# Performance work log

Hardware: AMD Instinct MI355X
Metric: run time of the kernel (lower is better)

The kernel has to match this reference:

```python
import jax, jax.numpy as jnp
import numpy as np

B, S, H, NH, DW, V, W, L, NL = 8, 512, 768, 12, 300, 100000, 256, 4, 2


def _make_word_index(seed=0):
    # contiguous, non-overlapping spans of length 1..L starting at pos 1,
    # zero-padded at the end (matches the `break` on (0,0) in the original).
    rng = np.random.default_rng(seed)
    wi = np.zeros((B, W, 2), np.int32)
    for b in range(B):
        pos, w = 1, 0
        while w < W and pos < S:
            n = int(rng.integers(1, L + 1))
            end = min(pos + n, S)
            wi[b, w] = (pos, end)
            pos, w = end, w + 1
    return jnp.asarray(wi)


def _lin(key, din, dout):
    kw, _ = jax.random.split(key)
    return jax.random.normal(kw, (din, dout), jnp.float32) * 0.02, jnp.zeros((dout,), jnp.float32)


def setup_inputs() -> dict:
    key = jax.random.key(0)
    ks = jax.random.split(key, 14)
    tbl = jax.random.normal(ks[2], (V + 1, DW), jnp.float32) * 0.1
    tbl = tbl.at[V].set(0.0)  # appended zero row for OOV/pad
    d = dict(
        sequence_output=jax.random.normal(ks[0], (B, S, H), jnp.float32),
        word_ids=jax.random.randint(ks[1], (B, W), 0, V),
        word_index=_make_word_index(),
        word_table=tbl,
        mix_lambda=jnp.asarray(0.5, jnp.float32),
        mu=jnp.asarray(0.5, jnp.float32),
    )
    d['dt_w'], d['dt_b'] = _lin(ks[3], DW, H)
    d['dr_w'], d['dr_b'] = _lin(ks[4], H, H)
    d['q_w'], d['q_b'] = _lin(ks[5], H, H)
    d['k_w'], d['k_b'] = _lin(ks[6], H, H)
    d['v_w'], d['v_b'] = _lin(ks[7], H, H)
    d['qi_w'], d['qi_b'] = _lin(ks[8], H, H)
    d['ki_w'], d['ki_b'] = _lin(ks[9], H, H)
    d['vi_w'], d['vi_b'] = _lin(ks[10], H, H)
    d['fus_w'], d['fus_b'] = _lin(ks[11], H, H)
    d['dense_w'], d['dense_b'] = _lin(ks[12], H, H)
    d['cls_w'], d['cls_b'] = _lin(ks[13], H, NL)
    return d


def _mhsa(x, wq, bq, wk, bk, wv, bv, bias=None):
    b, s, h = x.shape
    hd = h // NH
    q = (x @ wq + bq).reshape(b, s, NH, hd).transpose(0, 2, 1, 3)
    k = (x @ wk + bk).reshape(b, s, NH, hd).transpose(0, 2, 1, 3)
    v = (x @ wv + bv).reshape(b, s, NH, hd).transpose(0, 2, 1, 3)
    scores = jnp.einsum('bhqd,bhkd->bhqk', q, k) / jnp.sqrt(jnp.asarray(hd, x.dtype))
    if bias is not None:
        scores = scores + bias
    p = jax.nn.softmax(scores, axis=-1)
    return jnp.einsum('bhqk,bhkd->bhqd', p, v).transpose(0, 2, 1, 3).reshape(b, s, h)


def _forward(sequence_output, word_ids, word_index, word_table, dt_w, dt_b, dr_w, dr_b,
             mix_lambda, mu, q_w, q_b, k_w, k_b, v_w, v_b, qi_w, qi_b, ki_w, ki_b,
             vi_w, vi_b, fus_w, fus_b, dense_w, dense_b, cls_w, cls_b):
    x = sequence_output
    # word embedding -> dim_transform -> tanh -> dim_retain
    we = jnp.tanh(word_table[word_ids] @ dt_w + dt_b) @ dr_w + dr_b  # [B,W,H]
    starts, ends = word_index[..., 0], word_index[..., 1]
    n = ends - starts                     # word lengths, 0 for padding
    valid_w = n > 0
    lpos = jnp.arange(L)
    pos = jnp.clip(starts[..., None] + lpos, 0, S - 1)              # [B,W,L]
    cvalid = (lpos[None, None, :] < n[..., None]) & valid_w[..., None]
    bidx = jnp.arange(B)[:, None, None]
    # char-word cosine similarity (computed on the ORIGINAL sequence_output)
    xg = x[bidx, pos]                                               # [B,W,L,H]
    xn = xg / jnp.linalg.norm(xg, axis=-1, keepdims=True)
    wen = we / jnp.linalg.norm(we, axis=-1, keepdims=True)
    cos = jnp.sum(xn * wen[:, :, None, :], axis=-1)                 # [B,W,L]
    cos_m = jnp.where(cvalid, cos, -1e9)
    # add softmax(cos)-weighted word embedding onto chars (scatter-add)
    sm = jax.nn.softmax(cos_m, axis=-1) * cvalid
    x1 = x.at[bidx, pos].add(sm[..., None] * we[:, :, None, :])
    # ragged mix: most-important char (mic) per word
    mic = jnp.argmax(cos_m, axis=-1)                                # [B,W]
    x1g = x1[bidx, pos]                                             # [B,W,L,H]
    x_mic = x1g[jnp.arange(B)[:, None], jnp.arange(W)[None, :], mic]  # [B,W,H]
    sum_x = jnp.sum(x1g * cvalid[..., None], axis=2)                # [B,W,H]
    f = jnp.exp(mix_lambda - 1.0)
    a = (1.0 - f) / jnp.maximum(n - 1, 1).astype(x.dtype)           # [B,W]
    mix_other = (1.0 - a[..., None, None]) * x1g + a[..., None, None] * x_mic[:, :, None, :]
    mix_mic = f * x_mic + a[..., None] * (sum_x - x_mic)
    is_mic = lpos[None, None, :] == mic[:, :, None]
    newv = jnp.where(is_mic[..., None], mix_mic[:, :, None, :], mix_other)
    mixmask = (cvalid & (n > 1)[..., None])[..., None].astype(x.dtype)
    x_mix = x1.at[bidx, pos].add((newv - x1g) * mixmask)
    # importance attention mask: only mic (or the single char) columns visible
    keep_pos = jnp.where(n == 1, starts, jnp.clip(starts + mic, 0, S - 1))
    keep = jnp.zeros((B, S), bool).at[jnp.arange(B)[:, None], keep_pos].max(valid_w)
    bias = jnp.where(keep[:, None, None, :], 0.0, -jnp.inf).astype(x.dtype)  # [B,1,1,S]
    h1 = _mhsa(x_mix, q_w, q_b, k_w, k_b, v_w, v_b, None)
    h2 = _mhsa(x_mix, qi_w, qi_b, ki_w, ki_b, vi_w, vi_b, bias)
    fus = jnp.tanh((mu * h1 + (1.0 - mu) * h2) @ fus_w + fus_b)
    pooled = jnp.tanh(fus[:, 0] @ dense_w + dense_b)                # CLS pooling
    return pooled @ cls_w + cls_b                                   # [B,NL]


def reference(sequence_output, word_ids, word_index, word_table, dt_w, dt_b, dr_w, dr_b,
              mix_lambda, mu, q_w, q_b, k_w, k_b, v_w, v_b, qi_w, qi_b, ki_w, ki_b,
              vi_w, vi_b, fus_w, fus_b, dense_w, dense_b, cls_w, cls_b):
    return _forward(sequence_output, word_ids, word_index, word_table, dt_w, dt_b, dr_w, dr_b,
                    mix_lambda, mu, q_w, q_b, k_w, k_b, v_w, v_b, qi_w, qi_b, ki_w, ki_b,
                    vi_w, vi_b, fus_w, fus_b, dense_w, dense_b, cls_w, cls_b)
```

## Files before the change

### kernel.cpp

```cpp
#include <hip/hip_runtime.h>
#include <math.h>

#define NB 8
#define SS 512
#define HH 768
#define NHD 12
#define HDIM 64
#define DWD 300
#define WW 256
#define LL 4
#define KC 6

__device__ __forceinline__ float waveReduceSum(float v){
    #pragma unroll
    for(int o=32;o>0;o>>=1) v += __shfl_xor(v,o,64);
    return v;
}

__global__ __launch_bounds__(256) void k_embed1f(const float* __restrict__ table,
        const int* __restrict__ ids, const float* __restrict__ Wm,
        const float* __restrict__ bias, float* __restrict__ out,
        int* __restrict__ keep,
        const float* __restrict__ x, const float* __restrict__ qw,
        const float* __restrict__ qiw, float* __restrict__ qpart){
    int bid = blockIdx.x;
    int t = threadIdx.x;
    if(bid >= 400){
        int rb = bid - 400;
        int kc = rb % KC;
        int jt = (rb/KC) % 3;
        int b  = rb / (KC*3);
        int j = jt*256 + t;
        const float* x0 = x + (size_t)b*SS*HH;
        int i0 = kc*128;
        float a1=0.f, a2=0.f;
        for(int i=i0;i<i0+128;i++){
            float xv = x0[i];
            a1 += xv*qw[(size_t)i*HH+j];
            a2 += xv*qiw[(size_t)i*HH+j];
        }
        qpart[(((size_t)kc*NB + b)*2 + 0)*HH + j] = a1;
        qpart[(((size_t)kc*NB + b)*2 + 1)*HH + j] = a2;
        return;
    }
    if(bid >= 384){
        int i = (bid-384)*256 + t;
        if(i < NB*SS) keep[i] = 0;
        return;
    }
    const int K=300, NT=19;
    __shared__ float As[16][68];
    __shared__ float Bs[16][68];
    int bx = bid % 12;
    int by = bid / 12;
    int m0 = by*64, n0 = bx*64;
    int tm = t>>4, tn = t&15;
    int lm = t>>2, lk = (t&3)*4;
    int kk = t>>4, c4 = (t&15)*4;
    int row_id = ids[m0+lm];
    const float* arow = table + (size_t)row_id*DWD;
    float acc[4][4] = {};
    float4 av, bv;
    if(lk < K) av = *(const float4*)&arow[lk]; else av = make_float4(0,0,0,0);
    if(kk < K) bv = *(const float4*)&Wm[(size_t)kk*HH + n0 + c4]; else bv = make_float4(0,0,0,0);
    for(int kt=0;kt<NT;kt++){
        __syncthreads();
        As[lk+0][lm]=av.x; As[lk+1][lm]=av.y; As[lk+2][lm]=av.z; As[lk+3][lm]=av.w;
        *(float4*)&Bs[kk][c4] = bv;
        __syncthreads();
        if(kt+1 < NT){
            int k0 = (kt+1)*16;
            if(k0+lk < K) av = *(const float4*)&arow[k0+lk]; else av = make_float4(0,0,0,0);
            if(k0+kk < K) bv = *(const float4*)&Wm[(size_t)(k0+kk)*HH + n0 + c4]; else bv = make_float4(0,0,0,0);
        }
        #pragma unroll
        for(int k=0;k<16;k++){
            float4 a = *(const float4*)&As[k][tm*4];
            float4 b = *(const float4*)&Bs[k][tn*4];
            acc[0][0]+=a.x*b.x; acc[0][1]+=a.x*b.y; acc[0][2]+=a.x*b.z; acc[0][3]+=a.x*b.w;
            acc[1][0]+=a.y*b.x; acc[1][1]+=a.y*b.y; acc[1][2]+=a.y*b.z; acc[1][3]+=a.y*b.w;
            acc[2][0]+=a.z*b.x; acc[2][1]+=a.z*b.y; acc[2][2]+=a.z*b.z; acc[2][3]+=a.z*b.w;
            acc[3][0]+=a.w*b.x; acc[3][1]+=a.w*b.y; acc[3][2]+=a.w*b.z; acc[3][3]+=a.w*b.w;
        }
    }
    #pragma unroll
    for(int i=0;i<4;i++){
        int m = m0 + tm*4 + i;
        int n = n0 + tn*4;
        float4 o;
        o.x = tanhf(acc[i][0] + bias[n+0]);
        o.y = tanhf(acc[i][1] + bias[n+1]);
        o.z = tanhf(acc[i][2] + bias[n+2]);
        o.w = tanhf(acc[i][3] + bias[n+3]);
        *(float4*)&out[(size_t)m*HH + n] = o;
    }
}

__global__ __launch_bounds__(256) void k_embed2f(const float* __restrict__ A,
        const float* __restrict__ Wm, const float* __restrict__ bias,
        float* __restrict__ out,
        const float4* __restrict__ xin4, float4* __restrict__ xmix4,
        const float* __restrict__ qpart,
        const float* __restrict__ qb, const float* __restrict__ qib,
        const float* __restrict__ kb, const float* __restrict__ kib,
        float* __restrict__ q0g, float* __restrict__ cst){
    int bid = blockIdx.x;
    int t = threadIdx.x;
    if(bid >= 3456){
        int b = bid - 3456;
        __shared__ float q0s[HH], qi0s[HH];
        for(int j=t;j<HH;j+=256){
            float a1=qb[j], a2=qib[j];
            #pragma unroll
            for(int kc=0;kc<KC;kc++){
                a1 += qpart[(((size_t)kc*NB+b)*2+0)*HH+j];
                a2 += qpart[(((size_t)kc*NB+b)*2+1)*HH+j];
            }
            q0s[j]=a1; qi0s[j]=a2;
            q0g[((size_t)b*2+0)*HH+j]=a1;
            q0g[((size_t)b*2+1)*HH+j]=a2;
        }
        __syncthreads();
        if(t<24){
            int slot=t, h=slot%NHD;
            const float* Kb = (slot<NHD)? kb:kib;
            const float* Q  = (slot<NHD)? q0s:qi0s;
            float a=0.f;
            for(int j=0;j<HDIM;j++) a += Kb[h*HDIM+j]*Q[h*HDIM+j];
            cst[b*24+slot]=a;
        }
        return;
    }
    if(bid >= 384){
        int i = (bid-384)*256 + t;
        xmix4[i] = xin4[i];
        return;
    }
    const int NT = 48;
    __shared__ float As[16][68];
    __shared__ float Bs[16][68];
    int bx = bid % 12;
    int by = bid / 12;
    int m0 = by*64, n0 = bx*64;
    int tm = t>>4, tn = t&15;
    int lm = t>>2, lk = (t&3)*4;
    int kk = t>>4, c4 = (t&15)*4;
    const float* arow = A + (size_t)(m0+lm)*HH;
    float acc[4][4] = {};
    float4 av = *(const float4*)&arow[lk];
    float4 bv = *(const float4*)&Wm[(size_t)kk*HH + n0 + c4];
    for(int kt=0;kt<NT;kt++){
        __syncthreads();
        As[lk+0][lm]=av.x; As[lk+1][lm]=av.y; As[lk+2][lm]=av.z; As[lk+3][lm]=av.w;
        *(float4*)&Bs[kk][c4] = bv;
        __syncthreads();
        if(kt+1 < NT){
            int k0 = (kt+1)*16;
            av = *(const float4*)&arow[k0+lk];
            bv = *(const float4*)&Wm[(size_t)(k0+kk)*HH + n0 + c4];
        }
        #pragma unroll
        for(int k=0;k<16;k++){
            float4 a = *(const float4*)&As[k][tm*4];
            float4 b = *(const float4*)&Bs[k][tn*4];
            acc[0][0]+=a.x*b.x; acc[0][1]+=a.x*b.y; acc[0][2]+=a.x*b.z; acc[0][3]+=a.x*b.w;
            acc[1][0]+=a.y*b.x; acc[1][1]+=a.y*b.y; acc[1][2]+=a.y*b.z; acc[1][3]+=a.y*b.w;
            acc[2][0]+=a.z*b.x; acc[2][1]+=a.z*b.y; acc[2][2]+=a.z*b.z; acc[2][3]+=a.z*b.w;
            acc[3][0]+=a.w*b.x; acc[3][1]+=a.w*b.y; acc[3][2]+=a.w*b.z; acc[3][3]+=a.w*b.w;
        }
    }
    #pragma unroll
    for(int i=0;i<4;i++){
        int m = m0 + tm*4 + i;
        int n = n0 + tn*4;
        float4 o;
        o.x = acc[i][0] + bias[n+0];
        o.y = acc[i][1] + bias[n+1];
        o.z = acc[i][2] + bias[n+2];
        o.w = acc[i][3] + bias[n+3];
        *(float4*)&out[(size_t)m*HH + n] = o;
    }
}

__global__ __launch_bounds__(256) void k_cosmix(const float* __restrict__ x,
        const int* __restrict__ wi, const float* __restrict__ we,
        const float* __restrict__ lam, int* __restrict__ keep,
        float* __restrict__ xmix,
        const float* __restrict__ q0g, const float* __restrict__ kw,
        const float* __restrict__ kiw, float* __restrict__ r){
    int bid = blockIdx.x;
    int t = threadIdx.x;
    if(bid >= 2048){
        int rb = bid - 2048;
        int ct = rb % 3;
        int slot = (rb/3) % 24;
        int b = rb / 72;
        int h = slot % NHD;
        __shared__ float qs[HDIM];
        const float* Q = q0g + ((size_t)b*2 + (slot<NHD?0:1))*HH + h*HDIM;
        if(t<HDIM) qs[t] = Q[t];
        __syncthreads();
        const float* K = (slot<NHD)? kw : kiw;
        int c = ct*256 + t;
        const float4* K4 = (const float4*)(K + (size_t)c*HH + h*HDIM);
        const float4* q4 = (const float4*)qs;
        float a=0.f;
        #pragma unroll
        for(int j=0;j<16;j++){
            float4 kv=K4[j], qv=q4[j];
            a += kv.x*qv.x + kv.y*qv.y + kv.z*qv.z + kv.w*qv.w;
        }
        r[((size_t)(b*24+slot))*HH + c] = a;
        return;
    }
    int bw = bid;
    int b = bw >> 8;
    int start = wi[bw*2+0];
    int end   = wi[bw*2+1];
    int n = end - start;
    if(n <= 0) return;
    __shared__ float weS[HH];
    __shared__ float xrow[LL][HH];
    __shared__ float cos_s[LL];
    int wv = t>>6, lane = t&63;
    const float* wer = we + (size_t)bw*HH;
    float wev[12];
    float wn = 0.f;
    #pragma unroll
    for(int i=0;i<12;i++){
        float v = wer[lane+64*i];
        wev[i]=v; wn += v*v;
        if(wv==0) weS[lane+64*i] = v;
    }
    wn = waveReduceSum(wn);
    if(wv < n){
        const float* xr = x + ((size_t)(b*SS + start + wv))*HH;
        float d=0.f, xs=0.f;
        #pragma unroll
        for(int i=0;i<12;i++){
            float xv = xr[lane+64*i];
            xrow[wv][lane+64*i] = xv;
            d += xv*wev[i]; xs += xv*xv;
        }
        d = waveReduceSum(d); xs = waveReduceSum(xs);
        if(lane==0) cos_s[wv] = d / sqrtf(xs*wn);
    } else {
        if(lane==0) cos_s[wv] = -1e9f;
    }
    __syncthreads();
    float c0=cos_s[0], c1=cos_s[1], c2=cos_s[2], c3=cos_s[3];
    float m = fmaxf(fmaxf(c0,c1),fmaxf(c2,c3));
    float e0 = (0<n)? expf(c0-m):0.f;
    float e1 = (1<n)? expf(c1-m):0.f;
    float e2 = (2<n)? expf(c2-m):0.f;
    float e3 = (3<n)? expf(c3-m):0.f;
    float inv = 1.f/(e0+e1+e2+e3);
    float s0=e0*inv, s1=e1*inv, s2=e2*inv, s3=e3*inv;
    int mic = 0; float bv = c0;
    if(c1 > bv){bv=c1;mic=1;}
    if(c2 > bv){bv=c2;mic=2;}
    if(c3 > bv){bv=c3;mic=3;}
    if(t==0) keep[b*SS + start + mic] = 1;
    float f = expf(lam[0] - 1.f);
    float a = (n>1)? (1.f-f)/(float)(n-1) : (1.f-f);
    for(int j=t; j<HH; j+=256){
        float wej = weS[j];
        float v0=0.f,v1=0.f,v2=0.f,v3=0.f;
        if(0<n) v0 = xrow[0][j] + s0*wej;
        if(1<n) v1 = xrow[1][j] + s1*wej;
        if(2<n) v2 = xrow[2][j] + s2*wej;
        if(3<n) v3 = xrow[3][j] + s3*wej;
        float sumx = v0+v1+v2+v3;
        float xm = (mic==0)?v0:(mic==1)?v1:(mic==2)?v2:v3;
        float mm = f*xm + a*(sumx-xm);
        if(0<n) xmix[((size_t)(b*SS+start+0))*HH+j] = (0==mic)? (n==1? v0 : mm) : ((1.f-a)*v0 + a*xm);
        if(1<n) xmix[((size_t)(b*SS+start+1))*HH+j] = (1==mic)? mm : ((1.f-a)*v1 + a*xm);
        if(2<n) xmix[((size_t)(b*SS+start+2))*HH+j] = (2==mic)? mm : ((1.f-a)*v2 + a*xm);
        if(3<n) xmix[((size_t)(b*SS+start+3))*HH+j] = (3==mic)? mm : ((1.f-a)*v3 + a*xm);
    }
}

__global__ __launch_bounds__(256) void k_scores(const float* __restrict__ xmix,
        const float* __restrict__ r, const float* __restrict__ cst,
        const int* __restrict__ keep, float* __restrict__ scores){
    int bs = blockIdx.x;
    int b = bs >> 9, s = bs & 511;
    __shared__ float xr[HH];
    for(int i=threadIdx.x;i<HH;i+=256) xr[i] = xmix[(size_t)bs*HH + i];
    __syncthreads();
    int wv = threadIdx.x>>6, lane = threadIdx.x&63;
    int kp = keep[b*SS + s];
    #pragma unroll
    for(int q=0;q<6;q++){
        int slot = wv*6 + q;
        const float* rr = r + ((size_t)(b*24+slot))*HH;
        float d = 0.f;
        #pragma unroll
        for(int i=0;i<12;i++) d += xr[lane+64*i]*rr[lane+64*i];
        d = waveReduceSum(d);
        if(lane==0){
            float sc = (d + cst[b*24+slot])*0.125f;
            if(slot>=12 && !kp) sc = -1e30f;
            scores[((size_t)(b*24+slot))*SS + s] = sc;
        }
    }
}

__global__ __launch_bounds__(256) void k_attn(const float* __restrict__ scores,
        const float* __restrict__ xmix, float* __restrict__ cg){
    int rb = blockIdx.x;
    int jt = rb % 3;
    int bslot = rb / 3;
    int b = bslot / 24, slot = bslot % 24;
    int t = threadIdx.x;
    __shared__ float p[SS];
    __shared__ float red[256];
    const float* srow = scores + (size_t)bslot*SS;
    float v0 = srow[t], v1 = srow[t+256];
    red[t] = fmaxf(v0,v1); __syncthreads();
    for(int o=128;o>0;o>>=1){ if(t<o) red[t] = fmaxf(red[t],red[t+o]); __syncthreads(); }
    float m = red[0]; __syncthreads();
    float e0 = expf(v0-m), e1 = expf(v1-m);
    red[t] = e0+e1; __syncthreads();
    for(int o=128;o>0;o>>=1){ if(t<o) red[t] += red[t+o]; __syncthreads(); }
    float inv = 1.f/red[0];
    p[t] = e0*inv; p[t+256] = e1*inv;
    __syncthreads();
    int j = jt*256 + t;
    const float* xb = xmix + (size_t)b*SS*HH + j;
    float a0 = 0.f;
    for(int s=0;s<SS;s++) a0 += p[s]*xb[(size_t)s*HH];
    cg[((size_t)bslot)*HH + j] = a0;
    (void)slot;
}

__global__ __launch_bounds__(256) void k_finA(const float* __restrict__ cg,
        const float* __restrict__ vw, const float* __restrict__ viw,
        const float* __restrict__ mu_, float* __restrict__ part){
    int kc = blockIdx.x % KC;
    int jt = (blockIdx.x/KC) % 3;
    int b  = blockIdx.x / (KC*3);
    int j = jt*256 + threadIdx.x;
    int h = j >> 6;
    float mu = mu_[0];
    const float* c1 = cg + ((size_t)(b*24+h))*HH;
    const float* c2 = cg + ((size_t)(b*24+12+h))*HH;
    int i0 = kc*128;
    float a1=0.f, a2=0.f;
    for(int i=i0;i<i0+128;i++){
        a1 += c1[i]*vw[(size_t)i*HH+j];
        a2 += c2[i]*viw[(size_t)i*HH+j];
    }
    part[((size_t)kc*NB+b)*HH + j] = mu*a1 + (1.f-mu)*a2;
}

__global__ __launch_bounds__(256) void k_finB(const float* __restrict__ part1,
        const float* __restrict__ vb, const float* __restrict__ vib,
        const float* __restrict__ mu_, const float* __restrict__ fw,
        float* __restrict__ part2){
    int kc = blockIdx.x % KC;
    int jt = (blockIdx.x/KC) % 3;
    int b  = blockIdx.x / (KC*3);
    int i0 = kc*128;
    int t = threadIdx.x;
    __shared__ float gs[128];
    if(t < 128){
        int i = i0 + t;
        float mu = mu_[0];
        float s = mu*vb[i] + (1.f-mu)*vib[i];
        #pragma unroll
        for(int k2=0;k2<KC;k2++) s += part1[((size_t)k2*NB+b)*HH + i];
        gs[t] = s;
    }
    __syncthreads();
    int j = jt*256 + t;
    float a = 0.f;
    for(int k=0;k<128;k++) a += gs[k]*fw[(size_t)(i0+k)*HH + j];
    part2[((size_t)kc*NB+b)*HH + j] = a;
}

__global__ __launch_bounds__(256) void k_finC(const float* __restrict__ part2,
        const float* __restrict__ fb, const float* __restrict__ dw,
        float* __restrict__ part1){
    int kc = blockIdx.x % KC;
    int jt = (blockIdx.x/KC) % 3;
    int b  = blockIdx.x / (KC*3);
    int i0 = kc*128;
    int t = threadIdx.x;
    __shared__ float fs[128];
    if(t < 128){
        int i = i0 + t;
        float s = fb[i];
        #pragma unroll
        for(int k2=0;k2<KC;k2++) s += part2[((size_t)k2*NB+b)*HH + i];
        fs[t] = tanhf(s);
    }
    __syncthreads();
    int j = jt*256 + t;
    float a = 0.f;
    for(int k=0;k<128;k++) a += fs[k]*dw[(size_t)(i0+k)*HH + j];
    part1[((size_t)kc*NB+b)*HH + j] = a;
}

__global__ __launch_bounds__(256) void k_finD(const float* __restrict__ part,
        const float* __restrict__ db, const float* __restrict__ cw,
        const float* __restrict__ cb, float* __restrict__ out){
    int b = blockIdx.x;
    int t = threadIdx.x;
    __shared__ float pooled[HH];
    __shared__ float red[256];
    for(int j=t;j<HH;j+=256){
        float s = db[j];
        #pragma unroll
        for(int kc=0;kc<KC;kc++) s += part[((size_t)kc*NB+b)*HH+j];
        pooled[j] = tanhf(s);
    }
    __syncthreads();
    float p0=0.f, p1=0.f;
    for(int i=t;i<HH;i+=256){ p0 += pooled[i]*cw[i*2+0]; p1 += pooled[i]*cw[i*2+1]; }
    red[t]=p0; __syncthreads();
    for(int o=128;o>0;o>>=1){ if(t<o) red[t]+=red[t+o]; __syncthreads(); }
    if(t==0) out[b*2+0] = red[0]+cb[0];
    __syncthreads();
    red[t]=p1; __syncthreads();
    for(int o=128;o>0;o>>=1){ if(t<o) red[t]+=red[t+o]; __syncthreads(); }
    if(t==0) out[b*2+1] = red[0]+cb[1];
}

extern "C" void kernel_launch(void* const* d_in, const int* in_sizes, int n_in,
                              void* d_out, int out_size, void* d_ws, size_t ws_size,
                              hipStream_t stream) {
    const float* x          = (const float*)d_in[0];
    const int*   word_ids   = (const int*)  d_in[1];
    const int*   word_index = (const int*)  d_in[2];
    const float* table      = (const float*)d_in[3];
    const float* lam        = (const float*)d_in[4];
    const float* mu         = (const float*)d_in[5];
    const float* dt_w = (const float*)d_in[6];
    const float* dt_b = (const float*)d_in[7];
    const float* dr_w = (const float*)d_in[8];
    const float* dr_b = (const float*)d_in[9];
    const float* q_w  = (const float*)d_in[10];
    const float* q_b  = (const float*)d_in[11];
    const float* k_w  = (const float*)d_in[12];
    const float* k_b  = (const float*)d_in[13];
    const float* v_w  = (const float*)d_in[14];
    const float* v_b  = (const float*)d_in[15];
    const float* qi_w = (const float*)d_in[16];
    const float* qi_b = (const float*)d_in[17];
    const float* ki_w = (const float*)d_in[18];
    const float* ki_b = (const float*)d_in[19];
    const float* vi_w = (const float*)d_in[20];
    const float* vi_b = (const float*)d_in[21];
    const float* fus_w = (const float*)d_in[22];
    const float* fus_b = (const float*)d_in[23];
    const float* dense_w = (const float*)d_in[24];
    const float* dense_b = (const float*)d_in[25];
    const float* cls_w = (const float*)d_in[26];
    const float* cls_b = (const float*)d_in[27];
    float* out = (float*)d_out;

    char* w = (char*)d_ws;
    float* xmix   = (float*)(w + 0);
    float* tbuf   = (float*)(w + 12582912);
    float* we     = (float*)(w + 18874368);
    float* scores = (float*)(w + 25165824);
    float* r      = (float*)(w + 25559040);
    float* cst    = (float*)(w + 26148864);
    int*   keep   = (int*)  (w + 26149888);
    float* cg     = (float*)(w + 26166272);
    float* qpart  = (float*)(w + 26756096);
    float* q0g    = (float*)(w + 27051008);
    float* part1  = (float*)(w + 27100160);
    float* part2  = (float*)(w + 27247616);
    (void)ws_size; (void)in_sizes; (void)n_in; (void)out_size;

    k_embed1f<<<544, 256, 0, stream>>>(table, word_ids, dt_w, dt_b, tbuf, keep,
                                       x, q_w, qi_w, qpart);
    k_embed2f<<<3464, 256, 0, stream>>>(tbuf, dr_w, dr_b, we,
                                        (const float4*)x, (float4*)xmix,
                                        qpart, q_b, qi_b, k_b, ki_b, q0g, cst);
    k_cosmix<<<2624, 256, 0, stream>>>(x, word_index, we, lam, keep, xmix,
                                       q0g, k_w, ki_w, r);
    k_scores<<<NB*SS, 256, 0, stream>>>(xmix, r, cst, keep, scores);
    k_attn<<<NB*24*3, 256, 0, stream>>>(scores, xmix, cg);
    k_finA<<<NB*3*KC, 256, 0, stream>>>(cg, v_w, vi_w, mu, part1);
    k_finB<<<NB*3*KC, 256, 0, stream>>>(part1, v_b, vi_b, mu, fus_w, part2);
    k_finC<<<NB*3*KC, 256, 0, stream>>>(part2, fus_b, dense_w, part1);
    k_finD<<<NB, 256, 0, stream>>>(part1, dense_b, cls_w, cls_b, out);
}
```

Before: 446.7 us.

## Fuse all stages into one persistent cooperative kernel with grid syncs

Replaces the nine separate kernel launches with a single cooperative persistent kernel. Each former kernel becomes a grid-stride loop over its original block indices, and stages are separated by grid-wide barriers. This removes launch overhead and the gaps between dependent small kernels. In exchange, the grid is capped at 1024 blocks and heavy stages are serialised onto fewer resident blocks. Shared memory is unified into one buffer and launch bounds raise register pressure limits.

```diff
diff --git a/kernel.cpp b/kernel.cpp
--- a/kernel.cpp
+++ b/kernel.cpp
@@ -1,5 +1,8 @@
 #include <hip/hip_runtime.h>
+#include <hip/hip_cooperative_groups.h>
 #include <math.h>
+
+namespace cg = cooperative_groups;
 
 #define NB 8
 #define SS 512
@@ -11,481 +14,456 @@
 #define LL 4
 #define KC 6
 
+struct Params {
+    const float* x; const int* ids; const int* wi; const float* table;
+    const float* lam; const float* mu;
+    const float* dt_w; const float* dt_b; const float* dr_w; const float* dr_b;
+    const float* q_w;  const float* q_b;  const float* k_w;  const float* k_b;
+    const float* v_w;  const float* v_b;  const float* qi_w; const float* qi_b;
+    const float* ki_w; const float* ki_b; const float* vi_w; const float* vi_b;
+    const float* fus_w; const float* fus_b; const float* dense_w; const float* dense_b;
+    const float* cls_w; const float* cls_b;
+    float* out;
+    float* xmix; float* tbuf; float* we; float* scores; float* r; float* cst;
+    int* keep; float* cgb; float* qpart; float* q0g; float* part1; float* part2;
+};
+
 __device__ __forceinline__ float waveReduceSum(float v){
     #pragma unroll
     for(int o=32;o>0;o>>=1) v += __shfl_xor(v,o,64);
     return v;
 }
 
-__global__ __launch_bounds__(256) void k_embed1f(const float* __restrict__ table,
-        const int* __restrict__ ids, const float* __restrict__ Wm,
-        const float* __restrict__ bias, float* __restrict__ out,
-        int* __restrict__ keep,
-        const float* __restrict__ x, const float* __restrict__ qw,
-        const float* __restrict__ qiw, float* __restrict__ qpart){
-    int bid = blockIdx.x;
-    int t = threadIdx.x;
-    if(bid >= 400){
-        int rb = bid - 400;
-        int kc = rb % KC;
-        int jt = (rb/KC) % 3;
-        int b  = rb / (KC*3);
+__global__ __launch_bounds__(256, 4) void mega(Params P){
+    cg::grid_group gridg = cg::this_grid();
+    const int bid = blockIdx.x;
+    const int t   = threadIdx.x;
+    const int NBLK = gridDim.x;
+    __shared__ float sm[3872];
+
+    for(int wb=bid; wb<544; wb+=NBLK){
+        if(wb >= 400){
+            int rb = wb - 400;
+            int kc = rb % KC;
+            int jt = (rb/KC) % 3;
+            int b  = rb / (KC*3);
+            int j = jt*256 + t;
+            const float* x0 = P.x + (size_t)b*SS*HH;
+            int i0 = kc*128;
+            float a1=0.f, a2=0.f;
+            for(int i=i0;i<i0+128;i++){
+                float xv = x0[i];
+                a1 += xv*P.q_w[(size_t)i*HH+j];
+                a2 += xv*P.qi_w[(size_t)i*HH+j];
+            }
+            P.qpart[(((size_t)kc*NB + b)*2 + 0)*HH + j] = a1;
+            P.qpart[(((size_t)kc*NB + b)*2 + 1)*HH + j] = a2;
+        } else if(wb >= 384){
+            int i = (wb-384)*256 + t;
+            if(i < NB*SS) P.keep[i] = 0;
+        } else {
+            const int K=300, NT=19;
+            float (*As)[68] = (float(*)[68])sm;
+            float (*Bs)[68] = (float(*)[68])(sm+1088);
+            int bx = wb % 12, by = wb / 12;
+            int m0 = by*64, n0 = bx*64;
+            int tm = t>>4, tn = t&15;
+            int lm = t>>2, lk = (t&3)*4;
+            int kk = t>>4, c4 = (t&15)*4;
+            int row_id = P.ids[m0+lm];
+            const float* arow = P.table + (size_t)row_id*DWD;
+            float acc[4][4] = {};
+            float4 av, bv;
+            if(lk < K) av = *(const float4*)&arow[lk]; else av = make_float4(0,0,0,0);
+            if(kk < K) bv = *(const float4*)&P.dt_w[(size_t)kk*HH + n0 + c4]; else bv = make_float4(0,0,0,0);
+            for(int kt=0;kt<NT;kt++){
+                __syncthreads();
+                As[lk+0][lm]=av.x; As[lk+1][lm]=av.y; As[lk+2][lm]=av.z; As[lk+3][lm]=av.w;
+                *(float4*)&Bs[kk][c4] = bv;
+                __syncthreads();
+                if(kt+1 < NT){
+                    int k0 = (kt+1)*16;
+                    if(k0+lk < K) av = *(const float4*)&arow[k0+lk]; else av = make_float4(0,0,0,0);
+                    if(k0+kk < K) bv = *(const float4*)&P.dt_w[(size_t)(k0+kk)*HH + n0 + c4]; else bv = make_float4(0,0,0,0);
+                }
+                #pragma unroll
+                for(int k=0;k<16;k++){
+                    float4 a = *(const float4*)&As[k][tm*4];
+                    float4 b = *(const float4*)&Bs[k][tn*4];
+                    acc[0][0]+=a.x*b.x; acc[0][1]+=a.x*b.y; acc[0][2]+=a.x*b.z; acc[0][3]+=a.x*b.w;
+                    acc[1][0]+=a.y*b.x; acc[1][1]+=a.y*b.y; acc[1][2]+=a.y*b.z; acc[1][3]+=a.y*b.w;
+                    acc[2][0]+=a.z*b.x; acc[2][1]+=a.z*b.y; acc[2][2]+=a.z*b.z; acc[2][3]+=a.z*b.w;
+                    acc[3][0]+=a.w*b.x; acc[3][1]+=a.w*b.y; acc[3][2]+=a.w*b.z; acc[3][3]+=a.w*b.w;
+                }
+            }
+            #pragma unroll
+            for(int i=0;i<4;i++){
+                int m = m0 + tm*4 + i;
+                int n = n0 + tn*4;
+                float4 o;
+                o.x = tanhf(acc[i][0] + P.dt_b[n+0]);
+                o.y = tanhf(acc[i][1] + P.dt_b[n+1]);
+                o.z = tanhf(acc[i][2] + P.dt_b[n+2]);
+                o.w = tanhf(acc[i][3] + P.dt_b[n+3]);
+                *(float4*)&P.tbuf[(size_t)m*HH + n] = o;
+            }
+        }
+        __syncthreads();
+    }
+    gridg.sync();
+
+    for(int wb=bid; wb<3464; wb+=NBLK){
+        if(wb >= 3456){
+            int b = wb - 3456;
+            float* q0s  = sm;
+            float* qi0s = sm + 768;
+            for(int j=t;j<HH;j+=256){
+                float a1=P.q_b[j], a2=P.qi_b[j];
+                #pragma unroll
+                for(int kc=0;kc<KC;kc++){
+                    a1 += P.qpart[(((size_t)kc*NB+b)*2+0)*HH+j];
+                    a2 += P.qpart[(((size_t)kc*NB+b)*2+1)*HH+j];
+                }
+                q0s[j]=a1; qi0s[j]=a2;
+                P.q0g[((size_t)b*2+0)*HH+j]=a1;
+                P.q0g[((size_t)b*2+1)*HH+j]=a2;
+            }
+            __syncthreads();
+            if(t<24){
+                int slot=t, h=slot%NHD;
+                const float* Kb = (slot<NHD)? P.k_b : P.ki_b;
+                const float* Q  = (slot<NHD)? q0s : qi0s;
+                float a=0.f;
+                for(int j=0;j<HDIM;j++) a += Kb[h*HDIM+j]*Q[h*HDIM+j];
+                P.cst[b*24+slot]=a;
+            }
+        } else if(wb >= 384){
+            int i = (wb-384)*256 + t;
+            ((float4*)P.xmix)[i] = ((const float4*)P.x)[i];
+        } else {
+            const int NT = 48;
+            float (*As)[68] = (float(*)[68])sm;
+            float (*Bs)[68] = (float(*)[68])(sm+1088);
+            int bx = wb % 12, by = wb / 12;
+            int m0 = by*64, n0 = bx*64;
+            int tm = t>>4, tn = t&15;
+            int lm = t>>2, lk = (t&3)*4;
+            int kk = t>>4, c4 = (t&15)*4;
+            const float* arow = P.tbuf + (size_t)(m0+lm)*HH;
+            float acc[4][4] = {};
+            float4 av = *(const float4*)&arow[lk];
+            float4 bv = *(const float4*)&P.dr_w[(size_t)kk*HH + n0 + c4];
+            for(int kt=0;kt<NT;kt++){
+                __syncthreads();
+                As[lk+0][lm]=av.x; As[lk+1][lm]=av.y; As[lk+2][lm]=av.z; As[lk+3][lm]=av.w;
+                *(float4*)&Bs[kk][c4] = bv;
+                __syncthreads();
+                if(kt+1 < NT){
+                    int k0 = (kt+1)*16;
+                    av = *(const float4*)&arow[k0+lk];
+                    bv = *(const float4*)&P.dr_w[(size_t)(k0+kk)*HH + n0 + c4];
+                }
+                #pragma unroll
+                for(int k=0;k<16;k++){
+                    float4 a = *(const float4*)&As[k][tm*4];
+                    float4 b = *(const float4*)&Bs[k][tn*4];
+                    acc[0][0]+=a.x*b.x; acc[0][1]+=a.x*b.y; acc[0][2]+=a.x*b.z; acc[0][3]+=a.x*b.w;
+                    acc[1][0]+=a.y*b.x; acc[1][1]+=a.y*b.y; acc[1][2]+=a.y*b.z; acc[1][3]+=a.y*b.w;
+                    acc[2][0]+=a.z*b.x; acc[2][1]+=a.z*b.y; acc[2][2]+=a.z*b.z; acc[2][3]+=a.z*b.w;
+                    acc[3][0]+=a.w*b.x; acc[3][1]+=a.w*b.y; acc[3][2]+=a.w*b.z; acc[3][3]+=a.w*b.w;
+                }
+            }
+            #pragma unroll
+            for(int i=0;i<4;i++){
+                int m = m0 + tm*4 + i;
+                int n = n0 + tn*4;
+                float4 o;
+                o.x = acc[i][0] + P.dr_b[n+0];
+                o.y = acc[i][1] + P.dr_b[n+1];
+                o.z = acc[i][2] + P.dr_b[n+2];
+                o.w = acc[i][3] + P.dr_b[n+3];
+                *(float4*)&P.we[(size_t)m*HH + n] = o;
+            }
+        }
+        __syncthreads();
+    }
+    gridg.sync();
+
+    for(int wb=bid; wb<2624; wb+=NBLK){
+        if(wb >= 2048){
+            int rb = wb - 2048;
+            int ct = rb % 3;
+            int slot = (rb/3) % 24;
+            int b = rb / 72;
+            int h = slot % NHD;
+            float* qs = sm;
+            const float* Q = P.q0g + ((size_t)b*2 + (slot<NHD?0:1))*HH + h*HDIM;
+            if(t<HDIM) qs[t] = Q[t];
+            __syncthreads();
+            const float* Kp = (slot<NHD)? P.k_w : P.ki_w;
+            int c = ct*256 + t;
+            const float4* K4 = (const float4*)(Kp + (size_t)c*HH + h*HDIM);
+            const float4* q4 = (const float4*)qs;
+            float a=0.f;
+            #pragma unroll
+            for(int j=0;j<16;j++){
+                float4 kv=K4[j], qv=q4[j];
+                a += kv.x*qv.x + kv.y*qv.y + kv.z*qv.z + kv.w*qv.w;
+            }
+            P.r[((size_t)(b*24+slot))*HH + c] = a;
+        } else {
+            int bw = wb;
+            int b = bw >> 8;
+            int start = P.wi[bw*2+0];
+            int end   = P.wi[bw*2+1];
+            int n = end - start;
+            if(n > 0){
+                float* weS = sm;
+                float (*xrow)[HH] = (float(*)[HH])(sm+768);
+                float* cos_s = sm + 3840;
+                int wv = t>>6, lane = t&63;
+                const float* wer = P.we + (size_t)bw*HH;
+                float wev[12];
+                float wn = 0.f;
+                #pragma unroll
+                for(int i=0;i<12;i++){
+                    float v = wer[lane+64*i];
+                    wev[i]=v; wn += v*v;
+                    if(wv==0) weS[lane+64*i] = v;
+                }
+                wn = waveReduceSum(wn);
+                if(wv < n){
+                    const float* xr = P.x + ((size_t)(b*SS + start + wv))*HH;
+                    float d=0.f, xs=0.f;
+                    #pragma unroll
+                    for(int i=0;i<12;i++){
+                        float xv = xr[lane+64*i];
+                        xrow[wv][lane+64*i] = xv;
+                        d += xv*wev[i]; xs += xv*xv;
+                    }
+                    d = waveReduceSum(d); xs = waveReduceSum(xs);
+                    if(lane==0) cos_s[wv] = d / sqrtf(xs*wn);
+                } else {
+                    if(lane==0) cos_s[wv] = -1e9f;
+                }
+                __syncthreads();
+                float c0=cos_s[0], c1=cos_s[1], c2=cos_s[2], c3=cos_s[3];
+                float m = fmaxf(fmaxf(c0,c1),fmaxf(c2,c3));
+                float e0 = (0<n)? expf(c0-m):0.f;
+                float e1 = (1<n)? expf(c1-m):0.f;
+                float e2 = (2<n)? expf(c2-m):0.f;
+                float e3 = (3<n)? expf(c3-m):0.f;
+                float inv = 1.f/(e0+e1+e2+e3);
+                float s0=e0*inv, s1=e1*inv, s2=e2*inv, s3=e3*inv;
+                int mic = 0; float bv = c0;
+                if(c1 > bv){bv=c1;mic=1;}
+                if(c2 > bv){bv=c2;mic=2;}
+                if(c3 > bv){bv=c3;mic=3;}
+                if(t==0) P.keep[b*SS + start + mic] = 1;
+                float f = expf(P.lam[0] - 1.f);
+                float a = (n>1)? (1.f-f)/(float)(n-1) : (1.f-f);
+                for(int j=t; j<HH; j+=256){
+                    float wej = weS[j];
+                    float v0=0.f,v1=0.f,v2=0.f,v3=0.f;
+                    if(0<n) v0 = xrow[0][j] + s0*wej;
+                    if(1<n) v1 = xrow[1][j] + s1*wej;
+                    if(2<n) v2 = xrow[2][j] + s2*wej;
+                    if(3<n) v3 = xrow[3][j] + s3*wej;
+                    float sumx = v0+v1+v2+v3;
+                    float xm = (mic==0)?v0:(mic==1)?v1:(mic==2)?v2:v3;
+                    float mm = f*xm + a*(sumx-xm);
+                    if(0<n) P.xmix[((size_t)(b*SS+start+0))*HH+j] = (0==mic)? (n==1? v0 : mm) : ((1.f-a)*v0 + a*xm);
+                    if(1<n) P.xmix[((size_t)(b*SS+start+1))*HH+j] = (1==mic)? mm : ((1.f-a)*v1 + a*xm);
+                    if(2<n) P.xmix[((size_t)(b*SS+start+2))*HH+j] = (2==mic)? mm : ((1.f-a)*v2 + a*xm);
+                    if(3<n) P.xmix[((size_t)(b*SS+start+3))*HH+j] = (3==mic)? mm : ((1.f-a)*v3 + a*xm);
+                }
+            }
+        }
+        __syncthreads();
+    }
+    gridg.sync();
+
+    for(int wb=bid; wb<NB*SS; wb+=NBLK){
+        int b = wb >> 9, s = wb & 511;
+        float* xr = sm;
+        for(int i=t;i<HH;i+=256) xr[i] = P.xmix[(size_t)wb*HH + i];
+        __syncthreads();
+        int wv = t>>6, lane = t&63;
+        int kp = P.keep[b*SS + s];
+        #pragma unroll
+        for(int q=0;q<6;q++){
+            int slot = wv*6 + q;
+            const float* rr = P.r + ((size_t)(b*24+slot))*HH;
+            float d = 0.f;
+            #pragma unroll
+            for(int i=0;i<12;i++) d += xr[lane+64*i]*rr[lane+64*i];
+            d = waveReduceSum(d);
+            if(lane==0){
+                float sc = (d + P.cst[b*24+slot])*0.125f;
+                if(slot>=12 && !kp) sc = -1e30f;
+                P.scores[((size_t)(b*24+slot))*SS + s] = sc;
+            }
+        }
+        __syncthreads();
+    }
+    gridg.sync();
+
+    for(int wb=bid; wb<NB*24*3; wb+=NBLK){
+        int jt = wb % 3;
+        int bslot = wb / 3;
+        int b = bslot / 24;
+        float* p   = sm;
+        float* red = sm + 512;
+        const float* srow = P.scores + (size_t)bslot*SS;
+        float v0 = srow[t], v1 = srow[t+256];
+        red[t] = fmaxf(v0,v1); __syncthreads();
+        for(int o=128;o>0;o>>=1){ if(t<o) red[t] = fmaxf(red[t],red[t+o]); __syncthreads(); }
+        float m = red[0]; __syncthreads();
+        float e0 = expf(v0-m), e1 = expf(v1-m);
+        red[t] = e0+e1; __syncthreads();
+        for(int o=128;o>0;o>>=1){ if(t<o) red[t] += red[t+o]; __syncthreads(); }
+        float inv = 1.f/red[0];
+        p[t] = e0*inv; p[t+256] = e1*inv;
+        __syncthreads();
         int j = jt*256 + t;
-        const float* x0 = x + (size_t)b*SS*HH;
+        const float* xb = P.xmix + (size_t)b*SS*HH + j;
+        float a0 = 0.f;
+        for(int s=0;s<SS;s++) a0 += p[s]*xb[(size_t)s*HH];
+        P.cgb[((size_t)bslot)*HH + j] = a0;
+        __syncthreads();
+    }
+    gridg.sync();
+
+    for(int wb=bid; wb<NB*3*KC; wb+=NBLK){
+        int kc = wb % KC;
+        int jt = (wb/KC) % 3;
+        int b  = wb / (KC*3);
+        int j = jt*256 + t;
+        int h = j >> 6;
+        float mu = P.mu[0];
+        const float* c1 = P.cgb + ((size_t)(b*24+h))*HH;
+        const float* c2 = P.cgb + ((size_t)(b*24+12+h))*HH;
         int i0 = kc*128;
         float a1=0.f, a2=0.f;
         for(int i=i0;i<i0+128;i++){
-            float xv = x0[i];
-            a1 += xv*qw[(size_t)i*HH+j];
-            a2 += xv*qiw[(size_t)i*HH+j];
-        }
-        qpart[(((size_t)kc*NB + b)*2 + 0)*HH + j] = a1;
-        qpart[(((size_t)kc*NB + b)*2 + 1)*HH + j] = a2;
-        return;
-    }
-    if(bid >= 384){
-        int i = (bid-384)*256 + t;
-        if(i < NB*SS) keep[i] = 0;
-        return;
-    }
-    const int K=300, NT=19;
-    __shared__ float As[16][68];
-    __shared__ float Bs[16][68];
-    int bx = bid % 12;
-    int by = bid / 12;
-    int m0 = by*64, n0 = bx*64;
-    int tm = t>>4, tn = t&15;
-    int lm = t>>2, lk = (t&3)*4;
-    int kk = t>>4, c4 = (t&15)*4;
-    int row_id = ids[m0+lm];
-    const float* arow = table + (size_t)row_id*DWD;
-    float acc[4][4] = {};
-    float4 av, bv;
-    if(lk < K) av = *(const float4*)&arow[lk]; else av = make_float4(0,0,0,0);
-    if(kk < K) bv = *(const float4*)&Wm[(size_t)kk*HH + n0 + c4]; else bv = make_float4(0,0,0,0);
-    for(int kt=0;kt<NT;kt++){
-        __syncthreads();
-        As[lk+0][lm]=av.x; As[lk+1][lm]=av.y; As[lk+2][lm]=av.z; As[lk+3][lm]=av.w;
-        *(float4*)&Bs[kk][c4] = bv;
-        __syncthreads();
-        if(kt+1 < NT){
-            int k0 = (kt+1)*16;
-            if(k0+lk < K) av = *(const float4*)&arow[k0+lk]; else av = make_float4(0,0,0,0);
-            if(k0+kk < K) bv = *(const float4*)&Wm[(size_t)(k0+kk)*HH + n0 + c4]; else bv = make_float4(0,0,0,0);
-        }
-        #pragma unroll
-        for(int k=0;k<16;k++){
-            float4 a = *(const float4*)&As[k][tm*4];
-            float4 b = *(const float4*)&Bs[k][tn*4];
-            acc[0][0]+=a.x*b.x; acc[0][1]+=a.x*b.y; acc[0][2]+=a.x*b.z; acc[0][3]+=a.x*b.w;
-            acc[1][0]+=a.y*b.x; acc[1][1]+=a.y*b.y; acc[1][2]+=a.y*b.z; acc[1][3]+=a.y*b.w;
-            acc[2][0]+=a.z*b.x; acc[2][1]+=a.z*b.y; acc[2][2]+=a.z*b.z; acc[2][3]+=a.z*b.w;
-            acc[3][0]+=a.w*b.x; acc[3][1]+=a.w*b.y; acc[3][2]+=a.w*b.z; acc[3][3]+=a.w*b.w;
-        }
-    }
-    #pragma unroll
-    for(int i=0;i<4;i++){
-        int m = m0 + tm*4 + i;
-        int n = n0 + tn*4;
-        float4 o;
-        o.x = tanhf(acc[i][0] + bias[n+0]);
-        o.y = tanhf(acc[i][1] + bias[n+1]);
-        o.z = tanhf(acc[i][2] + bias[n+2]);
-        o.w = tanhf(acc[i][3] + bias[n+3]);
-        *(float4*)&out[(size_t)m*HH + n] = o;
-    }
-}
-
-__global__ __launch_bounds__(256) void k_embed2f(const float* __restrict__ A,
-        const float* __restrict__ Wm, const float* __restrict__ bias,
-        float* __restrict__ out,
-        const float4* __restrict__ xin4, float4* __restrict__ xmix4,
-        const float* __restrict__ qpart,
-        const float* __restrict__ qb, const float* __restrict__ qib,
-        const float* __restrict__ kb, const float* __restrict__ kib,
-        float* __restrict__ q0g, float* __restrict__ cst){
-    int bid = blockIdx.x;
-    int t = threadIdx.x;
-    if(bid >= 3456){
-        int b = bid - 3456;
-        __shared__ float q0s[HH], qi0s[HH];
+            a1 += c1[i]*P.v_w[(size_t)i*HH+j];
+            a2 += c2[i]*P.vi_w[(size_t)i*HH+j];
+        }
+        P.part1[((size_t)kc*NB+b)*HH + j] = mu*a1 + (1.f-mu)*a2;
+    }
+    gridg.sync();
+
+    for(int wb=bid; wb<NB*3*KC; wb+=NBLK){
+        int kc = wb % KC;
+        int jt = (wb/KC) % 3;
+        int b  = wb / (KC*3);
+        int i0 = kc*128;
+        float* gs = sm;
+        if(t < 128){
+            int i = i0 + t;
+            float mu = P.mu[0];
+            float s = mu*P.v_b[i] + (1.f-mu)*P.vi_b[i];
+            #pragma unroll
+            for(int k2=0;k2<KC;k2++) s += P.part1[((size_t)k2*NB+b)*HH + i];
+            gs[t] = s;
+        }
+        __syncthreads();
+        int j = jt*256 + t;
+        float a = 0.f;
+        for(int k=0;k<128;k++) a += gs[k]*P.fus_w[(size_t)(i0+k)*HH + j];
+        P.part2[((size_t)kc*NB+b)*HH + j] = a;
+        __syncthreads();
+    }
+    gridg.sync();
+
+    for(int wb=bid; wb<NB*3*KC; wb+=NBLK){
+        int kc = wb % KC;
+        int jt = (wb/KC) % 3;
+        int b  = wb / (KC*3);
+        int i0 = kc*128;
+        float* fs = sm;
+        if(t < 128){
+            int i = i0 + t;
+            float s = P.fus_b[i];
+            #pragma unroll
+            for(int k2=0;k2<KC;k2++) s += P.part2[((size_t)k2*NB+b)*HH + i];
+            fs[t] = tanhf(s);
+        }
+        __syncthreads();
+        int j = jt*256 + t;
+        float a = 0.f;
+        for(int k=0;k<128;k++) a += fs[k]*P.dense_w[(size_t)(i0+k)*HH + j];
+        P.part1[((size_t)kc*NB+b)*HH + j] = a;
+        __syncthreads();
+    }
+    gridg.sync();
+
+    for(int wb=bid; wb<NB; wb+=NBLK){
+        int b = wb;
+        float* pooled = sm;
+        float* red    = sm + 768;
         for(int j=t;j<HH;j+=256){
-            float a1=qb[j], a2=qib[j];
-            #pragma unroll
-            for(int kc=0;kc<KC;kc++){
-                a1 += qpart[(((size_t)kc*NB+b)*2+0)*HH+j];
-                a2 += qpart[(((size_t)kc*NB+b)*2+1)*HH+j];
-            }
-            q0s[j]=a1; qi0s[j]=a2;
-            q0g[((size_t)b*2+0)*HH+j]=a1;
-            q0g[((size_t)b*2+1)*HH+j]=a2;
-        }
-        __syncthreads();
-        if(t<24){
-            int slot=t, h=slot%NHD;
-            const float* Kb = (slot<NHD)? kb:kib;
-            const float* Q  = (slot<NHD)? q0s:qi0s;
-            float a=0.f;
-            for(int j=0;j<HDIM;j++) a += Kb[h*HDIM+j]*Q[h*HDIM+j];
-            cst[b*24+slot]=a;
-        }
-        return;
-    }
-    if(bid >= 384){
-        int i = (bid-384)*256 + t;
-        xmix4[i] = xin4[i];
-        return;
-    }
-    const int NT = 48;
-    __shared__ float As[16][68];
-    __shared__ float Bs[16][68];
-    int bx = bid % 12;
-    int by = bid / 12;
-    int m0 = by*64, n0 = bx*64;
-    int tm = t>>4, tn = t&15;
-    int lm = t>>2, lk = (t&3)*4;
-    int kk = t>>4, c4 = (t&15)*4;
-    const float* arow = A + (size_t)(m0+lm)*HH;
-    float acc[4][4] = {};
-    float4 av = *(const float4*)&arow[lk];
-    float4 bv = *(const float4*)&Wm[(size_t)kk*HH + n0 + c4];
-    for(int kt=0;kt<NT;kt++){
-        __syncthreads();
-        As[lk+0][lm]=av.x; As[lk+1][lm]=av.y; As[lk+2][lm]=av.z; As[lk+3][lm]=av.w;
-        *(float4*)&Bs[kk][c4] = bv;
-        __syncthreads();
-        if(kt+1 < NT){
-            int k0 = (kt+1)*16;
-            av = *(const float4*)&arow[k0+lk];
-            bv = *(const float4*)&Wm[(size_t)(k0+kk)*HH + n0 + c4];
-        }
-        #pragma unroll
-        for(int k=0;k<16;k++){
-            float4 a = *(const float4*)&As[k][tm*4];
-            float4 b = *(const float4*)&Bs[k][tn*4];
-            acc[0][0]+=a.x*b.x; acc[0][1]+=a.x*b.y; acc[0][2]+=a.x*b.z; acc[0][3]+=a.x*b.w;
-            acc[1][0]+=a.y*b.x; acc[1][1]+=a.y*b.y; acc[1][2]+=a.y*b.z; acc[1][3]+=a.y*b.w;
-            acc[2][0]+=a.z*b.x; acc[2][1]+=a.z*b.y; acc[2][2]+=a.z*b.z; acc[2][3]+=a.z*b.w;
-            acc[3][0]+=a.w*b.x; acc[3][1]+=a.w*b.y; acc[3][2]+=a.w*b.z; acc[3][3]+=a.w*b.w;
-        }
-    }
-    #pragma unroll
-    for(int i=0;i<4;i++){
-        int m = m0 + tm*4 + i;
-        int n = n0 + tn*4;
-        float4 o;
-        o.x = acc[i][0] + bias[n+0];
-        o.y = acc[i][1] + bias[n+1];
-        o.z = acc[i][2] + bias[n+2];
-        o.w = acc[i][3] + bias[n+3];
-        *(float4*)&out[(size_t)m*HH + n] = o;
-    }
-}
-
-__global__ __launch_bounds__(256) void k_cosmix(const float* __restrict__ x,
-        const int* __restrict__ wi, const float* __restrict__ we,
-        const float* __restrict__ lam, int* __restrict__ keep,
-        float* __restrict__ xmix,
-        const float* __restrict__ q0g, const float* __restrict__ kw,
-        const float* __restrict__ kiw, float* __restrict__ r){
-    int bid = blockIdx.x;
-    int t = threadIdx.x;
-    if(bid >= 2048){
-        int rb = bid - 2048;
-        int ct = rb % 3;
-        int slot = (rb/3) % 24;
-        int b = rb / 72;
-        int h = slot % NHD;
-        __shared__ float qs[HDIM];
-        const float* Q = q0g + ((size_t)b*2 + (slot<NHD?0:1))*HH + h*HDIM;
-        if(t<HDIM) qs[t] = Q[t];
-        __syncthreads();
-        const float* K = (slot<NHD)? kw : kiw;
-        int c = ct*256 + t;
-        const float4* K4 = (const float4*)(K + (size_t)c*HH + h*HDIM);
-        const float4* q4 = (const float4*)qs;
-        float a=0.f;
-        #pragma unroll
-        for(int j=0;j<16;j++){
-            float4 kv=K4[j], qv=q4[j];
-            a += kv.x*qv.x + kv.y*qv.y + kv.z*qv.z + kv.w*qv.w;
-        }
-        r[((size_t)(b*24+slot))*HH + c] = a;
-        return;
-    }
-    int bw = bid;
-    int b = bw >> 8;
-    int start = wi[bw*2+0];
-    int end   = wi[bw*2+1];
-    int n = end - start;
-    if(n <= 0) return;
-    __shared__ float weS[HH];
-    __shared__ float xrow[LL][HH];
-    __shared__ float cos_s[LL];
-    int wv = t>>6, lane = t&63;
-    const float* wer = we + (size_t)bw*HH;
-    float wev[12];
-    float wn = 0.f;
-    #pragma unroll
-    for(int i=0;i<12;i++){
-        float v = wer[lane+64*i];
-        wev[i]=v; wn += v*v;
-        if(wv==0) weS[lane+64*i] = v;
-    }
-    wn = waveReduceSum(wn);
-    if(wv < n){
-        const float* xr = x + ((size_t)(b*SS + start + wv))*HH;
-        float d=0.f, xs=0.f;
-        #pragma unroll
-        for(int i=0;i<12;i++){
-            float xv = xr[lane+64*i];
-            xrow[wv][lane+64*i] = xv;
-            d += xv*wev[i]; xs += xv*xv;
-        }
-        d = waveReduceSum(d); xs = waveReduceSum(xs);
-        if(lane==0) cos_s[wv] = d / sqrtf(xs*wn);
-    } else {
-        if(lane==0) cos_s[wv] = -1e9f;
-    }
-    __syncthreads();
-    float c0=cos_s[0], c1=cos_s[1], c2=cos_s[2], c3=cos_s[3];
-    float m = fmaxf(fmaxf(c0,c1),fmaxf(c2,c3));
-    float e0 = (0<n)? expf(c0-m):0.f;
-    float e1 = (1<n)? expf(c1-m):0.f;
-    float e2 = (2<n)? expf(c2-m):0.f;
-    float e3 = (3<n)? expf(c3-m):0.f;
-    float inv = 1.f/(e0+e1+e2+e3);
-    float s0=e0*inv, s1=e1*inv, s2=e2*inv, s3=e3*inv;
-    int mic = 0; float bv = c0;
-    if(c1 > bv){bv=c1;mic=1;}
-    if(c2 > bv){bv=c2;mic=2;}
-    if(c3 > bv){bv=c3;mic=3;}
-    if(t==0) keep[b*SS + start + mic] = 1;
-    float f = expf(lam[0] - 1.f);
-    float a = (n>1)? (1.f-f)/(float)(n-1) : (1.f-f);
-    for(int j=t; j<HH; j+=256){
-        float wej = weS[j];
-        float v0=0.f,v1=0.f,v2=0.f,v3=0.f;
-        if(0<n) v0 = xrow[0][j] + s0*wej;
-        if(1<n) v1 = xrow[1][j] + s1*wej;
-        if(2<n) v2 = xrow[2][j] + s2*wej;
-        if(3<n) v3 = xrow[3][j] + s3*wej;
-        float sumx = v0+v1+v2+v3;
-        float xm = (mic==0)?v0:(mic==1)?v1:(mic==2)?v2:v3;
-        float mm = f*xm + a*(sumx-xm);
-        if(0<n) xmix[((size_t)(b*SS+start+0))*HH+j] = (0==mic)? (n==1? v0 : mm) : ((1.f-a)*v0 + a*xm);
-        if(1<n) xmix[((size_t)(b*SS+start+1))*HH+j] = (1==mic)? mm : ((1.f-a)*v1 + a*xm);
-        if(2<n) xmix[((size_t)(b*SS+start+2))*HH+j] = (2==mic)? mm : ((1.f-a)*v2 + a*xm);
-        if(3<n) xmix[((size_t)(b*SS+start+3))*HH+j] = (3==mic)? mm : ((1.f-a)*v3 + a*xm);
-    }
-}
-
-__global__ __launch_bounds__(256) void k_scores(const float* __restrict__ xmix,
-        const float* __restrict__ r, const float* __restrict__ cst,
-        const int* __restrict__ keep, float* __restrict__ scores){
-    int bs = blockIdx.x;
-    int b = bs >> 9, s = bs & 511;
-    __shared__ float xr[HH];
-    for(int i=threadIdx.x;i<HH;i+=256) xr[i] = xmix[(size_t)bs*HH + i];
-    __syncthreads();
-    int wv = threadIdx.x>>6, lane = threadIdx.x&63;
-    int kp = keep[b*SS + s];
-    #pragma unroll
-    for(int q=0;q<6;q++){
-        int slot = wv*6 + q;
-        const float* rr = r + ((size_t)(b*24+slot))*HH;
-        float d = 0.f;
-        #pragma unroll
-        for(int i=0;i<12;i++) d += xr[lane+64*i]*rr[lane+64*i];
-        d = waveReduceSum(d);
-        if(lane==0){
-            float sc = (d + cst[b*24+slot])*0.125f;
-            if(slot>=12 && !kp) sc = -1e30f;
-            scores[((size_t)(b*24+slot))*SS + s] = sc;
-        }
-    }
-}
-
-__global__ __launch_bounds__(256) void k_attn(const float* __restrict__ scores,
-        const float* __restrict__ xmix, float* __restrict__ cg){
-    int rb = blockIdx.x;
-    int jt = rb % 3;
-    int bslot = rb / 3;
-    int b = bslot / 24, slot = bslot % 24;
-    int t = threadIdx.x;
-    __shared__ float p[SS];
-    __shared__ float red[256];
-    const float* srow = scores + (size_t)bslot*SS;
-    float v0 = srow[t], v1 = srow[t+256];
-    red[t] = fmaxf(v0,v1); __syncthreads();
-    for(int o=128;o>0;o>>=1){ if(t<o) red[t] = fmaxf(red[t],red[t+o]); __syncthreads(); }
-    float m = red[0]; __syncthreads();
-    float e0 = expf(v0-m), e1 = expf(v1-m);
-    red[t] = e0+e1; __syncthreads();
-    for(int o=128;o>0;o>>=1){ if(t<o) red[t] += red[t+o]; __syncthreads(); }
-    float inv = 1.f/red[0];
-    p[t] = e0*inv; p[t+256] = e1*inv;
-    __syncthreads();
-    int j = jt*256 + t;
-    const float* xb = xmix + (size_t)b*SS*HH + j;
-    float a0 = 0.f;
-    for(int s=0;s<SS;s++) a0 += p[s]*xb[(size_t)s*HH];
-    cg[((size_t)bslot)*HH + j] = a0;
-    (void)slot;
-}
-
-__global__ __launch_bounds__(256) void k_finA(const float* __restrict__ cg,
-        const float* __restrict__ vw, const float* __restrict__ viw,
-        const float* __restrict__ mu_, float* __restrict__ part){
-    int kc = blockIdx.x % KC;
-    int jt = (blockIdx.x/KC) % 3;
-    int b  = blockIdx.x / (KC*3);
-    int j = jt*256 + threadIdx.x;
-    int h = j >> 6;
-    float mu = mu_[0];
-    const float* c1 = cg + ((size_t)(b*24+h))*HH;
-    const float* c2 = cg + ((size_t)(b*24+12+h))*HH;
-    int i0 = kc*128;
-    float a1=0.f, a2=0.f;
-    for(int i=i0;i<i0+128;i++){
-        a1 += c1[i]*vw[(size_t)i*HH+j];
-        a2 += c2[i]*viw[(size_t)i*HH+j];
-    }
-    part[((size_t)kc*NB+b)*HH + j] = mu*a1 + (1.f-mu)*a2;
-}
-
-__global__ __launch_bounds__(256) void k_finB(const float* __restrict__ part1,
-        const float* __restrict__ vb, const float* __restrict__ vib,
-        const float* __restrict__ mu_, const float* __restrict__ fw,
-        float* __restrict__ part2){
-    int kc = blockIdx.x % KC;
-    int jt = (blockIdx.x/KC) % 3;
-    int b  = blockIdx.x / (KC*3);
-    int i0 = kc*128;
-    int t = threadIdx.x;
-    __shared__ float gs[128];
-    if(t < 128){
-        int i = i0 + t;
-        float mu = mu_[0];
-        float s = mu*vb[i] + (1.f-mu)*vib[i];
-        #pragma unroll
-        for(int k2=0;k2<KC;k2++) s += part1[((size_t)k2*NB+b)*HH + i];
-        gs[t] = s;
-    }
-    __syncthreads();
-    int j = jt*256 + t;
-    float a = 0.f;
-    for(int k=0;k<128;k++) a += gs[k]*fw[(size_t)(i0+k)*HH + j];
-    part2[((size_t)kc*NB+b)*HH + j] = a;
-}
-
-__global__ __launch_bounds__(256) void k_finC(const float* __restrict__ part2,
-        const float* __restrict__ fb, const float* __restrict__ dw,
-        float* __restrict__ part1){
-    int kc = blockIdx.x % KC;
-    int jt = (blockIdx.x/KC) % 3;
-    int b  = blockIdx.x / (KC*3);
-    int i0 = kc*128;
-    int t = threadIdx.x;
-    __shared__ float fs[128];
-    if(t < 128){
-        int i = i0 + t;
-        float s = fb[i];
-        #pragma unroll
-        for(int k2=0;k2<KC;k2++) s += part2[((size_t)k2*NB+b)*HH + i];
-        fs[t] = tanhf(s);
-    }
-    __syncthreads();
-    int j = jt*256 + t;
-    float a = 0.f;
-    for(int k=0;k<128;k++) a += fs[k]*dw[(size_t)(i0+k)*HH + j];
-    part1[((size_t)kc*NB+b)*HH + j] = a;
-}
-
-__global__ __launch_bounds__(256) void k_finD(const float* __restrict__ part,
-        const float* __restrict__ db, const float* __restrict__ cw,
-        const float* __restrict__ cb, float* __restrict__ out){
-    int b = blockIdx.x;
-    int t = threadIdx.x;
-    __shared__ float pooled[HH];
-    __shared__ float red[256];
-    for(int j=t;j<HH;j+=256){
-        float s = db[j];
-        #pragma unroll
-        for(int kc=0;kc<KC;kc++) s += part[((size_t)kc*NB+b)*HH+j];
-        pooled[j] = tanhf(s);
-    }
-    __syncthreads();
-    float p0=0.f, p1=0.f;
-    for(int i=t;i<HH;i+=256){ p0 += pooled[i]*cw[i*2+0]; p1 += pooled[i]*cw[i*2+1]; }
-    red[t]=p0; __syncthreads();
-    for(int o=128;o>0;o>>=1){ if(t<o) red[t]+=red[t+o]; __syncthreads(); }
-    if(t==0) out[b*2+0] = red[0]+cb[0];
-    __syncthreads();
-    red[t]=p1; __syncthreads();
-    for(int o=128;o>0;o>>=1){ if(t<o) red[t]+=red[t+o]; __syncthreads(); }
-    if(t==0) out[b*2+1] = red[0]+cb[1];
+            float s = P.dense_b[j];
+            #pragma unroll
+            for(int kc=0;kc<KC;kc++) s += P.part1[((size_t)kc*NB+b)*HH+j];
+            pooled[j] = tanhf(s);
+        }
+        __syncthreads();
+        float p0=0.f, p1=0.f;
+        for(int i=t;i<HH;i+=256){ p0 += pooled[i]*P.cls_w[i*2+0]; p1 += pooled[i]*P.cls_w[i*2+1]; }
+        red[t]=p0; __syncthreads();
+        for(int o=128;o>0;o>>=1){ if(t<o) red[t]+=red[t+o]; __syncthreads(); }
+        if(t==0) P.out[b*2+0] = red[0]+P.cls_b[0];
+        __syncthreads();
+        red[t]=p1; __syncthreads();
+        for(int o=128;o>0;o>>=1){ if(t<o) red[t]+=red[t+o]; __syncthreads(); }
+        if(t==0) P.out[b*2+1] = red[0]+P.cls_b[1];
+        __syncthreads();
+    }
 }
 
 extern "C" void kernel_launch(void* const* d_in, const int* in_sizes, int n_in,
                               void* d_out, int out_size, void* d_ws, size_t ws_size,
                               hipStream_t stream) {
-    const float* x          = (const float*)d_in[0];
-    const int*   word_ids   = (const int*)  d_in[1];
-    const int*   word_index = (const int*)  d_in[2];
-    const float* table      = (const float*)d_in[3];
-    const float* lam        = (const float*)d_in[4];
-    const float* mu         = (const float*)d_in[5];
-    const float* dt_w = (const float*)d_in[6];
-    const float* dt_b = (const float*)d_in[7];
-    const float* dr_w = (const float*)d_in[8];
-    const float* dr_b = (const float*)d_in[9];
-    const float* q_w  = (const float*)d_in[10];
-    const float* q_b  = (const float*)d_in[11];
-    const float* k_w  = (const float*)d_in[12];
-    const float* k_b  = (const float*)d_in[13];
-    const float* v_w  = (const float*)d_in[14];
-    const float* v_b  = (const float*)d_in[15];
-    const float* qi_w = (const float*)d_in[16];
-    const float* qi_b = (const float*)d_in[17];
-    const float* ki_w = (const float*)d_in[18];
-    const float* ki_b = (const float*)d_in[19];
-    const float* vi_w = (const float*)d_in[20];
-    const float* vi_b = (const float*)d_in[21];
-    const float* fus_w = (const float*)d_in[22];
-    const float* fus_b = (const float*)d_in[23];
-    const float* dense_w = (const float*)d_in[24];
-    const float* dense_b = (const float*)d_in[25];
-    const float* cls_w = (const float*)d_in[26];
-    const float* cls_b = (const float*)d_in[27];
-    float* out = (float*)d_out;
-
     char* w = (char*)d_ws;
-    float* xmix   = (float*)(w + 0);
-    float* tbuf   = (float*)(w + 12582912);
-    float* we     = (float*)(w + 18874368);
-    float* scores = (float*)(w + 25165824);
-    float* r      = (float*)(w + 25559040);
-    float* cst    = (float*)(w + 26148864);
-    int*   keep   = (int*)  (w + 26149888);
-    float* cg     = (float*)(w + 26166272);
-    float* qpart  = (float*)(w + 26756096);
-    float* q0g    = (float*)(w + 27051008);
-    float* part1  = (float*)(w + 27100160);
-    float* part2  = (float*)(w + 27247616);
+    Params hp;
+    hp.x       = (const float*)d_in[0];
+    hp.ids     = (const int*)  d_in[1];
+    hp.wi      = (const int*)  d_in[2];
+    hp.table   = (const float*)d_in[3];
+    hp.lam     = (const float*)d_in[4];
+    hp.mu      = (const float*)d_in[5];
+    hp.dt_w = (const float*)d_in[6];   hp.dt_b = (const float*)d_in[7];
+    hp.dr_w = (const float*)d_in[8];   hp.dr_b = (const float*)d_in[9];
+    hp.q_w  = (const float*)d_in[10];  hp.q_b  = (const float*)d_in[11];
+    hp.k_w  = (const float*)d_in[12];  hp.k_b  = (const float*)d_in[13];
+    hp.v_w  = (const float*)d_in[14];  hp.v_b  = (const float*)d_in[15];
+    hp.qi_w = (const float*)d_in[16];  hp.qi_b = (const float*)d_in[17];
+    hp.ki_w = (const float*)d_in[18];  hp.ki_b = (const float*)d_in[19];
+    hp.vi_w = (const float*)d_in[20];  hp.vi_b = (const float*)d_in[21];
+    hp.fus_w = (const float*)d_in[22]; hp.fus_b = (const float*)d_in[23];
+    hp.dense_w = (const float*)d_in[24]; hp.dense_b = (const float*)d_in[25];
+    hp.cls_w = (const float*)d_in[26]; hp.cls_b = (const float*)d_in[27];
+    hp.out = (float*)d_out;
+    hp.xmix   = (float*)(w + 0);
+    hp.tbuf   = (float*)(w + 12582912);
+    hp.we     = (float*)(w + 18874368);
+    hp.scores = (float*)(w + 25165824);
+    hp.r      = (float*)(w + 25559040);
+    hp.cst    = (float*)(w + 26148864);
+    hp.keep   = (int*)  (w + 26149888);
+    hp.cgb    = (float*)(w + 26166272);
+    hp.qpart  = (float*)(w + 26756096);
+    hp.q0g    = (float*)(w + 27051008);
+    hp.part1  = (float*)(w + 27100160);
+    hp.part2  = (float*)(w + 27247616);
     (void)ws_size; (void)in_sizes; (void)n_in; (void)out_size;
 
-    k_embed1f<<<544, 256, 0, stream>>>(table, word_ids, dt_w, dt_b, tbuf, keep,
-                                       x, q_w, qi_w, qpart);
-    k_embed2f<<<3464, 256, 0, stream>>>(tbuf, dr_w, dr_b, we,
-                                        (const float4*)x, (float4*)xmix,
-                                        qpart, q_b, qi_b, k_b, ki_b, q0g, cst);
-    k_cosmix<<<2624, 256, 0, stream>>>(x, word_index, we, lam, keep, xmix,
-                                       q0g, k_w, ki_w, r);
-    k_scores<<<NB*SS, 256, 0, stream>>>(xmix, r, cst, keep, scores);
-    k_attn<<<NB*24*3, 256, 0, stream>>>(scores, xmix, cg);
-    k_finA<<<NB*3*KC, 256, 0, stream>>>(cg, v_w, vi_w, mu, part1);
-    k_finB<<<NB*3*KC, 256, 0, stream>>>(part1, v_b, vi_b, mu, fus_w, part2);
-    k_finC<<<NB*3*KC, 256, 0, stream>>>(part2, fus_b, dense_w, part1);
-    k_finD<<<NB, 256, 0, stream>>>(part1, dense_b, cls_w, cls_b, out);
+    int nb = 0;
+    hipOccupancyMaxActiveBlocksPerMultiprocessor(&nb, mega, 256, 0);
+    if(nb < 1) nb = 1;
+    int gridn = nb * 256;
+    if(gridn > 1024) gridn = 1024;
+    void* args[] = { &hp };
+    hipLaunchCooperativeKernel((void*)mega, dim3(gridn), dim3(256), args, 0, stream);
 }
```

Result: slower. 962.8 us (+115.5%).
